# Kernel optimization log

Hardware: AMD Instinct MI355X
Metric: run time of the kernel (lower is better)

The kernel has to match this reference:

```python
import jax, jax.numpy as jnp
import numpy as np

DIM_MODEL = 1024
NUM_HEADS = 16
HEAD_DIM = DIM_MODEL // NUM_HEADS
NEG = -1000000000.0


def setup_inputs() -> dict:
    key = jax.random.key(0)
    ks = jax.random.split(key, 11)
    B, S, D = 2, 2048, DIM_MODEL
    s = 1.0 / np.sqrt(D)
    return {
        "q": jax.random.normal(ks[0], (B, S, D), jnp.float32),
        "k": jax.random.normal(ks[1], (B, S, D), jnp.float32),
        "v": jax.random.normal(ks[2], (B, S, D), jnp.float32),
        "Wq": jax.random.normal(ks[3], (D, D), jnp.float32) * s,
        "bq": jnp.zeros((D,), jnp.float32),
        "Wk": jax.random.normal(ks[4], (D, D), jnp.float32) * s,
        "bk": jnp.zeros((D,), jnp.float32),
        "Wv": jax.random.normal(ks[5], (D, D), jnp.float32) * s,
        "bv": jnp.zeros((D,), jnp.float32),
        "Wo": jax.random.normal(ks[6], (D, D), jnp.float32) * s,
        "bo": jnp.zeros((D,), jnp.float32),
    }


def reference(q, k, v, Wq, bq, Wk, bk, Wv, bv, Wo, bo):
    B, S, D = q.shape
    H, hd = NUM_HEADS, HEAD_DIM

    def proj(x, W, b):
        # torch Linear: x @ W.T + b, then split heads -> [B, H, S, hd]
        y = jnp.einsum("bsd,ed->bse", x, W) + b
        return y.reshape(B, S, H, hd).transpose(0, 2, 1, 3)

    qh = proj(q, Wq, bq)
    kh = proj(k, Wk, bk)
    vh = proj(v, Wv, bv)

    scores = jnp.einsum("bhqd,bhkd->bhqk", qh, kh) / np.sqrt(hd)
    # torch.triu(ones(S,S), diagonal=0): upper triangle INCLUDING diagonal is masked
    mask = jnp.triu(jnp.ones((S, S), bool))
    scores = jnp.where(mask, NEG, scores)
    # softmax over dim=-2 (query axis), as in the original module
    attn = jax.nn.softmax(scores, axis=-2)
    ctx = jnp.einsum("bhqk,bhkd->bhqd", attn, vh)  # [B,H,S,hd]
    ctx = ctx.transpose(0, 2, 1, 3).reshape(B, S, D)
    return jnp.einsum("bsd,ed->bse", ctx, Wo) + bo
```

## Files before the change

### kernel.cpp

```cpp
#include <hip/hip_runtime.h>

typedef __bf16 bf16;
typedef __attribute__((ext_vector_type(8))) __bf16 bf16x8;
typedef __attribute__((ext_vector_type(2))) __bf16 bf16x2;
typedef __attribute__((ext_vector_type(4))) float f32x4;

#define AS1 __attribute__((address_space(1)))
#define AS3 __attribute__((address_space(3)))

#define BB 2
#define SS 2048
#define DD 1024
#define HH 16
#define HD 64
#define BH (BB*HH)

#define QSCALE 0.1803368801111244f

static __device__ __forceinline__ f32x4 mfma16(bf16x8 a, bf16x8 b, f32x4 c) {
  return __builtin_amdgcn_mfma_f32_16x16x32_bf16(a, b, c, 0, 0, 0);
}
static __device__ __forceinline__ float fexp2(float x) {
  return __builtin_amdgcn_exp2f(x);
}

static __device__ __forceinline__ void swz1024(int bid, int& bh, int& strip0, int& qh) {
  int c = bid & 7, j = bid >> 3;
  bh = c + 8 * (j & 3);
  int rem = j >> 2;
  strip0 = rem & 15;
  qh = rem >> 4;
}

__global__ __launch_bounds__(256) void cvt_w(const float* __restrict__ s0, const float* __restrict__ s1,
                                             const float* __restrict__ s2, const float* __restrict__ s3,
                                             bf16* __restrict__ o0, bf16* __restrict__ o1,
                                             bf16* __restrict__ o2, bf16* __restrict__ o3) {
  const int z = blockIdx.y;
  const float* s = (z == 0) ? s0 : (z == 1) ? s1 : (z == 2) ? s2 : s3;
  bf16* o = (z == 0) ? o0 : (z == 1) ? o1 : (z == 2) ? o2 : o3;
  int i = blockIdx.x * 256 + threadIdx.x;
  const float4* sp = (const float4*)s;
  float4 a = sp[2 * i], b = sp[2 * i + 1];
  bf16x8 v;
  v[0] = (bf16)a.x; v[1] = (bf16)a.y; v[2] = (bf16)a.z; v[3] = (bf16)a.w;
  v[4] = (bf16)b.x; v[5] = (bf16)b.y; v[6] = (bf16)b.z; v[7] = (bf16)b.w;
  ((bf16x8*)o)[i] = v;
}

__global__ __launch_bounds__(256) void cvt_x(const float* __restrict__ s0, const float* __restrict__ s1,
                                             const float* __restrict__ s2,
                                             bf16* __restrict__ o0, bf16* __restrict__ o1,
                                             bf16* __restrict__ o2) {
  const int z = blockIdx.y;
  const float* s = (z == 0) ? s0 : (z == 1) ? s1 : s2;
  bf16* o = (z == 0) ? o0 : (z == 1) ? o1 : o2;
  int i = blockIdx.x * 256 + threadIdx.x;
  const float4* sp = (const float4*)s;
  float4 a = sp[2 * i], b = sp[2 * i + 1];
  bf16x8 v;
  v[0] = (bf16)a.x; v[1] = (bf16)a.y; v[2] = (bf16)a.z; v[3] = (bf16)a.w;
  v[4] = (bf16)b.x; v[5] = (bf16)b.y; v[6] = (bf16)b.z; v[7] = (bf16)b.w;
  ((bf16x8*)o)[i] = v;
}

__device__ __forceinline__ void gemm_core(const bf16* __restrict__ A,
                                          const bf16* __restrict__ Bm, int K,
                                          int m0, int n0, int w, int l,
                                          bf16* sA, bf16* sB, f32x4 (&acc)[4][4]) {
  const int l15 = l & 15, lg = l >> 4;
  const int wr = (w >> 1) * 64, wc = (w & 1) * 64;
  for (int kt = 0; kt < K; kt += 32) {
#pragma unroll
    for (int i = 0; i < 2; ++i) {
      int t = i * 256 + w * 64 + l;
      const bf16* ga = A + (size_t)(m0 + (t >> 2)) * K + kt + (t & 3) * 8;
      const bf16* gb = Bm + (size_t)(n0 + (t >> 2)) * K + kt + (t & 3) * 8;
      __builtin_amdgcn_global_load_lds((const AS1 void*)ga,
                                       (AS3 void*)(sA + (i * 256 + w * 64) * 8), 16, 0, 0);
      __builtin_amdgcn_global_load_lds((const AS1 void*)gb,
                                       (AS3 void*)(sB + (i * 256 + w * 64) * 8), 16, 0, 0);
    }
    __syncthreads();
    bf16x8 af[4], bfr[4];
#pragma unroll
    for (int m = 0; m < 4; ++m)
      af[m] = *(const bf16x8*)(sA + (wr + m * 16 + l15) * 32 + lg * 8);
#pragma unroll
    for (int n = 0; n < 4; ++n)
      bfr[n] = *(const bf16x8*)(sB + (wc + n * 16 + l15) * 32 + lg * 8);
#pragma unroll
    for (int m = 0; m < 4; ++m)
#pragma unroll
      for (int n = 0; n < 4; ++n)
        acc[m][n] = mfma16(af[m], bfr[n], acc[m][n]);
    __syncthreads();
  }
}

__global__ __launch_bounds__(256) void proj_gemm(
    const bf16* __restrict__ Xq, const bf16* __restrict__ Xk, const bf16* __restrict__ Xv,
    const bf16* __restrict__ Wq, const bf16* __restrict__ Wk, const bf16* __restrict__ Wv,
    const float* __restrict__ bq, const float* __restrict__ bk, const float* __restrict__ bv,
    bf16* __restrict__ Oq, bf16* __restrict__ Ok, bf16* __restrict__ Ovt) {
  __shared__ __align__(16) bf16 sA[128 * 32];
  __shared__ __align__(16) bf16 sB[128 * 32];
  const int z = blockIdx.z;
  const bf16* A = (z == 0) ? Xq : ((z == 1) ? Xk : Xv);
  const bf16* W = (z == 0) ? Wq : ((z == 1) ? Wk : Wv);
  const float* bias = (z == 0) ? bq : ((z == 1) ? bk : bv);
  const int tid = threadIdx.x, l = tid & 63, w = tid >> 6;
  const int m0 = blockIdx.y * 128, n0 = blockIdx.x * 128;
  f32x4 acc[4][4] = {};
  gemm_core(A, W, DD, m0, n0, w, l, sA, sB, acc);
  const int l15 = l & 15, lg = l >> 4;
  const int wr = (w >> 1) * 64, wc = (w & 1) * 64;
#pragma unroll
  for (int n = 0; n < 4; ++n) {
    int col = n0 + wc + n * 16 + l15;
    float bb = bias[col];
    int h = col >> 6, d = col & 63;
#pragma unroll
    for (int m = 0; m < 4; ++m) {
#pragma unroll
      for (int r = 0; r < 4; ++r) {
        int row = m0 + wr + m * 16 + lg * 4 + r;
        int b = row >> 11, s = row & (SS - 1);
        float vv = acc[m][n][r] + bb;
        if (z == 0) vv *= QSCALE;
        if (z != 2)
          ((z == 0) ? Oq : Ok)[(((size_t)(b * HH + h)) * SS + s) * HD + d] = (bf16)vv;
        else
          Ovt[(size_t)(b * HH + h) * SS * HD + ((s >> 5) * 64 + d) * 32 + (s & 31)] = (bf16)vv;
      }
    }
  }
}

__global__ __launch_bounds__(256) void out_gemm(const bf16* __restrict__ A,
                                                const bf16* __restrict__ W,
                                                const float* __restrict__ bias,
                                                float* __restrict__ out) {
  __shared__ __align__(16) bf16 sA[128 * 32];
  __shared__ __align__(16) bf16 sB[128 * 32];
  const int tid = threadIdx.x, l = tid & 63, w = tid >> 6;
  const int m0 = blockIdx.y * 128, n0 = blockIdx.x * 128;
  f32x4 acc[4][4] = {};
  gemm_core(A, W, DD, m0, n0, w, l, sA, sB, acc);
  const int l15 = l & 15, lg = l >> 4;
  const int wr = (w >> 1) * 64, wc = (w & 1) * 64;
#pragma unroll
  for (int n = 0; n < 4; ++n) {
    int col = n0 + wc + n * 16 + l15;
    float bb = bias[col];
#pragma unroll
    for (int m = 0; m < 4; ++m)
#pragma unroll
      for (int r = 0; r < 4; ++r) {
        int row = m0 + wr + m * 16 + lg * 4 + r;
        out[(size_t)row * DD + col] = acc[m][n][r] + bb;
      }
  }
}

__global__ __launch_bounds__(256) void colz(const bf16* __restrict__ Qb,
                                            const bf16* __restrict__ Kb,
                                            float* __restrict__ zPart) {
  __shared__ float zred[4][64];
  int bh, pair, qh;
  swz1024(blockIdx.x, bh, pair, qh);
  const int tid = threadIdx.x, l = tid & 63, w = tid >> 6;
  const int l15 = l & 15, lg = l >> 4;
  const bf16* Q = Qb + (size_t)bh * SS * HD;
  const bf16* Kh = Kb + (size_t)bh * SS * HD;

  for (int half = 0; half < 2; ++half) {
    const int s = half ? (31 - pair) : pair;
    const int c0 = s * 64;
    bf16x8 kf[4][2];
#pragma unroll
    for (int kt = 0; kt < 4; ++kt) {
      kf[kt][0] = *(const bf16x8*)&Kh[(c0 + kt * 16 + l15) * HD + lg * 8];
      kf[kt][1] = *(const bf16x8*)&Kh[(c0 + kt * 16 + l15) * HD + 32 + lg * 8];
    }
    float z[4] = {};
    const int qstart = c0 + qh * 64 + w * 16;
    bf16x8 qa0, qa1, qn0, qn1;
    if (qstart < SS) {
      qa0 = *(const bf16x8*)&Q[(qstart + l15) * HD + lg * 8];
      qa1 = *(const bf16x8*)&Q[(qstart + l15) * HD + 32 + lg * 8];
    }
    for (int qb = qstart; qb < SS; qb += 128) {
      const int qnext = qb + 128;
      if (qnext < SS) {
        qn0 = *(const bf16x8*)&Q[(qnext + l15) * HD + lg * 8];
        qn1 = *(const bf16x8*)&Q[(qnext + l15) * HD + 32 + lg * 8];
      }
      f32x4 d[4] = {};
#pragma unroll
      for (int kt = 0; kt < 4; ++kt) {
        d[kt] = mfma16(qa0, kf[kt][0], d[kt]);
        d[kt] = mfma16(qa1, kf[kt][1], d[kt]);
      }
#pragma unroll
      for (int kt = 0; kt < 4; ++kt) {
        const int kcol = c0 + kt * 16 + l15;
#pragma unroll
        for (int r = 0; r < 4; ++r) {
          int qq = qb + lg * 4 + r;
          z[kt] += (qq > kcol) ? fexp2(d[kt][r]) : 0.f;
        }
      }
      qa0 = qn0; qa1 = qn1;
    }
#pragma unroll
    for (int kt = 0; kt < 4; ++kt) {
      z[kt] += __shfl_xor(z[kt], 16);
      z[kt] += __shfl_xor(z[kt], 32);
    }
    if (l < 16) {
#pragma unroll
      for (int kt = 0; kt < 4; ++kt) zred[w][kt * 16 + l15] = z[kt];
    }
    __syncthreads();
    if (tid < 64) {
      float zs = zred[0][tid] + zred[1][tid] + zred[2][tid] + zred[3][tid];
      zPart[((size_t)qh * BH + bh) * SS + c0 + tid] = zs;
    }
    __syncthreads();
  }
}

__global__ __launch_bounds__(256) void rzfin(const float* __restrict__ zPart,
                                             float* __restrict__ cRZ) {
  int i = blockIdx.x * 256 + threadIdx.x;
  f32x4 a = ((const f32x4*)zPart)[i];
  f32x4 b = ((const f32x4*)(zPart + (size_t)BH * SS))[i];
  f32x4 r;
#pragma unroll
  for (int j = 0; j < 4; ++j) {
    float s = a[j] + b[j];
    r[j] = (s > 0.f) ? 1.0f / s : 0.f;
  }
  ((f32x4*)cRZ)[i] = r;
}

__global__ __launch_bounds__(256) void vscale(bf16* __restrict__ Vt,
                                              const float* __restrict__ cRZ,
                                              float* __restrict__ vlastB) {
  int i = blockIdx.x * 256 + threadIdx.x;
  int ks8 = i & 3;
  int d = (i >> 2) & 63;
  int ts = (i >> 8) & 63;
  int bh = i >> 14;
  bf16* p = Vt + ((((size_t)bh * 64 + ts) * 64 + d) * 32) + ks8 * 8;
  const float* rz = cRZ + (size_t)bh * SS + ts * 32 + ks8 * 8;
  bf16x8 v = *(const bf16x8*)p;
  if (ts == 63 && ks8 == 3) vlastB[bh * 64 + d] = (float)v[7] * (1.0f / (float)SS);
  f32x4 r0 = *(const f32x4*)rz, r1 = *(const f32x4*)(rz + 4);
  bf16x8 o;
#pragma unroll
  for (int j = 0; j < 4; ++j) o[j] = (bf16)((float)v[j] * r0[j]);
#pragma unroll
  for (int j = 0; j < 4; ++j) o[4 + j] = (bf16)((float)v[4 + j] * r1[j]);
  *(bf16x8*)p = o;
}

struct KV {
  bf16x8 k[4];
  unsigned int v[4][4];
};

static __device__ __forceinline__ void kv_load(KV& b, const bf16* __restrict__ Kh,
                                               const bf16* __restrict__ V, int k0,
                                               int l15, int lg) {
  b.k[0] = *(const bf16x8*)&Kh[(k0 + l15) * HD + lg * 8];
  b.k[1] = *(const bf16x8*)&Kh[(k0 + l15) * HD + 32 + lg * 8];
  b.k[2] = *(const bf16x8*)&Kh[(k0 + 16 + l15) * HD + lg * 8];
  b.k[3] = *(const bf16x8*)&Kh[(k0 + 16 + l15) * HD + 32 + lg * 8];
  const bf16* tile = V + ((size_t)(k0 >> 5) << 11);
#pragma unroll
  for (int dt = 0; dt < 4; ++dt) {
    const bf16* base = tile + (dt * 16 + l15) * 32;
    uint2 lo = *(const uint2*)&base[4 * lg];
    uint2 hi = *(const uint2*)&base[16 + 4 * lg];
    b.v[dt][0] = lo.x; b.v[dt][1] = lo.y; b.v[dt][2] = hi.x; b.v[dt][3] = hi.y;
  }
}

template <bool DIAG>
static __device__ __forceinline__ void kv_compute(const KV& b, int k0, int q0,
                                                  const bf16x8 (&qa)[4][2],
                                                  f32x4 (&acc)[4][4], int l15, int lg) {
  const int kb0i = k0 + lg * 4, kb1i = k0 + 16 + lg * 4;
#pragma unroll
  for (int qt = 0; qt < 4; ++qt) {
    f32x4 s0 = {}, s1 = {};
    s0 = mfma16(b.k[0], qa[qt][0], s0);
    s0 = mfma16(b.k[1], qa[qt][1], s0);
    s1 = mfma16(b.k[2], qa[qt][0], s1);
    s1 = mfma16(b.k[3], qa[qt][1], s1);
    const int qq = q0 + qt * 16 + l15;
    union { unsigned int u[4]; bf16x8 v; } pa;
#pragma unroll
    for (int hw = 0; hw < 2; ++hw) {
      bf16x2 t0, t1;
#pragma unroll
      for (int r = 0; r < 2; ++r) {
        int rr = hw * 2 + r;
        float p0 = fexp2(s0[rr]);
        float p1 = fexp2(s1[rr]);
        if (DIAG) {
          p0 = (kb0i + rr < qq) ? p0 : 0.f;
          p1 = (kb1i + rr < qq) ? p1 : 0.f;
        }
        t0[r] = (bf16)p0;
        t1[r] = (bf16)p1;
      }
      pa.u[hw] = __builtin_bit_cast(unsigned int, t0);
      pa.u[hw + 2] = __builtin_bit_cast(unsigned int, t1);
    }
#pragma unroll
    for (int dt = 0; dt < 4; ++dt) {
      union { unsigned int u[4]; bf16x8 v; } vf;
      vf.u[0] = b.v[dt][0]; vf.u[1] = b.v[dt][1];
      vf.u[2] = b.v[dt][2]; vf.u[3] = b.v[dt][3];
      acc[qt][dt] = mfma16(pa.v, vf.v, acc[qt][dt]);
    }
  }
}

__global__ __launch_bounds__(256, 2) void attn_ctx(const bf16* __restrict__ Qb,
                                                   const bf16* __restrict__ Kb,
                                                   const bf16* __restrict__ Vt,
                                                   bf16* __restrict__ ctxP0,
                                                   bf16* __restrict__ ctxP1) {
  __shared__ __align__(16) float red[2][64 * 68];
  int bh, pr, kh;
  swz1024(blockIdx.x, bh, pr, kh);
  const int tid = threadIdx.x, l = tid & 63, w = tid >> 6;
  const int l15 = l & 15, lg = l >> 4;
  const int s = kh * 4 + w;
  const bf16* Q = Qb + (size_t)bh * SS * HD;
  const bf16* Kh = Kb + (size_t)bh * SS * HD;
  const bf16* V = Vt + (size_t)bh * SS * HD;
  bf16* ctxP = kh ? ctxP1 : ctxP0;
  const int b = bh >> 4, h = bh & 15;

  for (int half = 0; half < 2; ++half) {
    const int t = half ? (31 - pr) : pr;
    const int q0 = t * 64;

    bf16x8 qa[4][2];
#pragma unroll
    for (int qt = 0; qt < 4; ++qt)
#pragma unroll
      for (int kk = 0; kk < 2; ++kk)
        qa[qt][kk] = *(const bf16x8*)&Q[(q0 + qt * 16 + l15) * HD + kk * 32 + lg * 8];

    f32x4 acc[4][4] = {};
    KV A;
    for (int k0 = s * 32; k0 < q0; k0 += 256) {
      kv_load(A, Kh, V, k0, l15, lg);
      kv_compute<false>(A, k0, q0, qa, acc, l15, lg);
    }
    {
      const int cw = (2 * t) & 7;
      int dk = (s == cw) ? q0 : ((s == ((cw + 1) & 7)) ? q0 + 32 : -1);
      if (dk >= 0) {
        kv_load(A, Kh, V, dk, l15, lg);
        kv_compute<true>(A, dk, q0, qa, acc, l15, lg);
      }
    }

    if (w == 1 || w == 3) {
      float* buf = red[(w - 1) >> 1];
#pragma unroll
      for (int qt = 0; qt < 4; ++qt)
#pragma unroll
        for (int dt = 0; dt < 4; ++dt)
          *(f32x4*)&buf[(dt * 16 + l15) * 68 + qt * 16 + lg * 4] = acc[qt][dt];
    }
    __syncthreads();
    if (w == 0 || w == 2) {
      const float* buf = red[w >> 1];
#pragma unroll
      for (int qt = 0; qt < 4; ++qt)
#pragma unroll
        for (int dt = 0; dt < 4; ++dt)
          acc[qt][dt] += *(const f32x4*)&buf[(dt * 16 + l15) * 68 + qt * 16 + lg * 4];
    }
    __syncthreads();
    if (w == 2) {
#pragma unroll
      for (int qt = 0; qt < 4; ++qt)
#pragma unroll
        for (int dt = 0; dt < 4; ++dt)
          *(f32x4*)&red[0][(dt * 16 + l15) * 68 + qt * 16 + lg * 4] = acc[qt][dt];
    }
    __syncthreads();
    if (w == 0) {
#pragma unroll
      for (int qt = 0; qt < 4; ++qt) {
#pragma unroll
        for (int dt = 0; dt < 4; ++dt) {
          f32x4 a = acc[qt][dt];
          a += *(const f32x4*)&red[0][(dt * 16 + l15) * 68 + qt * 16 + lg * 4];
#pragma unroll
          for (int r = 0; r < 4; ++r) {
            int q = q0 + qt * 16 + lg * 4 + r;
            ctxP[((size_t)(b * SS + q)) * DD + h * HD + dt * 16 + l15] = (bf16)a[r];
          }
        }
      }
    }
    __syncthreads();
  }
}

__global__ __launch_bounds__(256) void ctxfin(const bf16* __restrict__ P1,
                                              const float* __restrict__ vlastB,
                                              bf16* __restrict__ ctx) {
  int i = blockIdx.x * 256 + threadIdx.x;
  int e0 = i * 8;
  int row = e0 >> 10, col = e0 & (DD - 1);
  int b = row >> 11;
  int vidx = (b * HH + (col >> 6)) * 64 + (col & 63);
  bf16x8 p0 = ((const bf16x8*)ctx)[i];
  bf16x8 p1 = ((const bf16x8*)P1)[i];
  f32x4 v0 = *(const f32x4*)&vlastB[vidx];
  f32x4 v1 = *(const f32x4*)&vlastB[vidx + 4];
  bf16x8 o;
#pragma unroll
  for (int j = 0; j < 4; ++j) o[j] = (bf16)((float)p0[j] + (float)p1[j] + v0[j]);
#pragma unroll
  for (int j = 0; j < 4; ++j) o[4 + j] = (bf16)((float)p0[4 + j] + (float)p1[4 + j] + v1[j]);
  ((bf16x8*)ctx)[i] = o;
}

extern "C" void kernel_launch(void* const* d_in, const int* in_sizes, int n_in,
                              void* d_out, int out_size, void* d_ws, size_t ws_size,
                              hipStream_t stream) {
  const float* q  = (const float*)d_in[0];
  const float* k  = (const float*)d_in[1];
  const float* v  = (const float*)d_in[2];
  const float* Wq = (const float*)d_in[3];
  const float* bq = (const float*)d_in[4];
  const float* Wk = (const float*)d_in[5];
  const float* bk = (const float*)d_in[6];
  const float* Wv = (const float*)d_in[7];
  const float* bv = (const float*)d_in[8];
  const float* Wo = (const float*)d_in[9];
  const float* bo = (const float*)d_in[10];

  char* ws = (char*)d_ws;
  const size_t SZP = (size_t)4096 * 1024 * 2;
  const size_t SZW = (size_t)1024 * 1024 * 2;
  bf16* Qb   = (bf16*)(ws + 0 * SZP);
  bf16* Kb   = (bf16*)(ws + 1 * SZP);
  bf16* Vt   = (bf16*)(ws + 2 * SZP);
  bf16* ctxb = (bf16*)(ws + 3 * SZP);
  bf16* qb16 = (bf16*)(ws + 4 * SZP);
  bf16* kb16 = (bf16*)(ws + 5 * SZP);
  bf16* vb16 = (bf16*)(ws + 6 * SZP);
  bf16* Wqb  = (bf16*)(ws + 7 * SZP + 0 * SZW);
  bf16* Wkb  = (bf16*)(ws + 7 * SZP + 1 * SZW);
  bf16* Wvb  = (bf16*)(ws + 7 * SZP + 2 * SZW);
  bf16* Wob  = (bf16*)(ws + 7 * SZP + 3 * SZW);
  float* zPart = (float*)(ws + 7 * SZP + 4 * SZW);
  float* cRZ   = zPart + (size_t)2 * BH * SS;
  float* vlastB = cRZ + (size_t)BH * SS;
  bf16* ctxP1 = qb16;

  cvt_w<<<dim3(512, 4), 256, 0, stream>>>(Wq, Wk, Wv, Wo, Wqb, Wkb, Wvb, Wob);
  cvt_x<<<dim3(2048, 3), 256, 0, stream>>>(q, k, v, qb16, kb16, vb16);

  proj_gemm<<<dim3(1024 / 128, 4096 / 128, 3), 256, 0, stream>>>(
      qb16, kb16, vb16, Wqb, Wkb, Wvb, bq, bk, bv, Qb, Kb, Vt);

  colz<<<1024, 256, 0, stream>>>(Qb, Kb, zPart);
  rzfin<<<(BH * SS / 4) / 256, 256, 0, stream>>>(zPart, cRZ);
  vscale<<<(BH * HD * SS / 8) / 256, 256, 0, stream>>>(Vt, cRZ, vlastB);
  attn_ctx<<<1024, 256, 0, stream>>>(Qb, Kb, Vt, ctxb, ctxP1);
  ctxfin<<<(4096 * 1024 / 8) / 256, 256, 0, stream>>>(ctxP1, vlastB, ctxb);

  out_gemm<<<dim3(1024 / 128, 4096 / 128), 256, 0, stream>>>(ctxb, Wob, bo, (float*)d_out);
}
```

Before: 168.2 us.

## Share K/V chunks via LDS across waves and split keys four ways

The attention kernel changes from per-wave private K/V register loads with a shared-memory cross-wave reduction to a 128-query tile. Each wave owns 32 query rows, and the block stages each 32-key K/V chunk into LDS with global_load_lds so all four waves reuse it. The key range is now split across four blocks instead of two, writing four partial context buffers that ctxfin sums. This removes the LDS reduction and cuts redundant global K/V loads. In exchange it adds two barriers per chunk, one more partial buffer to write and read, and reuses the kb16/vb16 scratch buffers as partial outputs.

Result: no change. 169.3 us (+0.7%).

```diff
diff --git a/kernel.cpp b/kernel.cpp
--- a/kernel.cpp
+++ b/kernel.cpp
@@ -24,12 +24,12 @@
   return __builtin_amdgcn_exp2f(x);
 }
 
-static __device__ __forceinline__ void swz1024(int bid, int& bh, int& strip0, int& qh) {
+static __device__ __forceinline__ void swz1024(int bid, int& bh, int& a, int& b2) {
   int c = bid & 7, j = bid >> 3;
   bh = c + 8 * (j & 3);
   int rem = j >> 2;
-  strip0 = rem & 15;
-  qh = rem >> 4;
+  a = rem & 15;
+  b2 = rem >> 4;
 }
 
 __global__ __launch_bounds__(256) void cvt_w(const float* __restrict__ s0, const float* __restrict__ s1,
@@ -266,42 +266,33 @@
   *(bf16x8*)p = o;
 }
 
-struct KV {
-  bf16x8 k[4];
-  unsigned int v[4][4];
-};
-
-static __device__ __forceinline__ void kv_load(KV& b, const bf16* __restrict__ Kh,
-                                               const bf16* __restrict__ V, int k0,
-                                               int l15, int lg) {
-  b.k[0] = *(const bf16x8*)&Kh[(k0 + l15) * HD + lg * 8];
-  b.k[1] = *(const bf16x8*)&Kh[(k0 + l15) * HD + 32 + lg * 8];
-  b.k[2] = *(const bf16x8*)&Kh[(k0 + 16 + l15) * HD + lg * 8];
-  b.k[3] = *(const bf16x8*)&Kh[(k0 + 16 + l15) * HD + 32 + lg * 8];
-  const bf16* tile = V + ((size_t)(k0 >> 5) << 11);
+template <bool DIAG>
+static __device__ __forceinline__ void chunk_compute(
+    const bf16* sKe, const bf16* sVe, int k0, int qw,
+    const bf16x8 (&qa)[2][2], f32x4 (&acc)[2][4], int l15, int lg) {
+  bf16x8 kf00 = *(const bf16x8*)(sKe + l15 * 32 + lg * 8);
+  bf16x8 kf01 = *(const bf16x8*)(sKe + 1024 + l15 * 32 + lg * 8);
+  bf16x8 kf10 = *(const bf16x8*)(sKe + (16 + l15) * 32 + lg * 8);
+  bf16x8 kf11 = *(const bf16x8*)(sKe + 1024 + (16 + l15) * 32 + lg * 8);
+  union U { unsigned int u[4]; bf16x8 v; };
+  U vf[4];
 #pragma unroll
   for (int dt = 0; dt < 4; ++dt) {
-    const bf16* base = tile + (dt * 16 + l15) * 32;
+    const bf16* base = sVe + (dt * 16 + l15) * 32;
     uint2 lo = *(const uint2*)&base[4 * lg];
     uint2 hi = *(const uint2*)&base[16 + 4 * lg];
-    b.v[dt][0] = lo.x; b.v[dt][1] = lo.y; b.v[dt][2] = hi.x; b.v[dt][3] = hi.y;
-  }
-}
-
-template <bool DIAG>
-static __device__ __forceinline__ void kv_compute(const KV& b, int k0, int q0,
-                                                  const bf16x8 (&qa)[4][2],
-                                                  f32x4 (&acc)[4][4], int l15, int lg) {
+    vf[dt].u[0] = lo.x; vf[dt].u[1] = lo.y; vf[dt].u[2] = hi.x; vf[dt].u[3] = hi.y;
+  }
   const int kb0i = k0 + lg * 4, kb1i = k0 + 16 + lg * 4;
 #pragma unroll
-  for (int qt = 0; qt < 4; ++qt) {
+  for (int qt = 0; qt < 2; ++qt) {
     f32x4 s0 = {}, s1 = {};
-    s0 = mfma16(b.k[0], qa[qt][0], s0);
-    s0 = mfma16(b.k[1], qa[qt][1], s0);
-    s1 = mfma16(b.k[2], qa[qt][0], s1);
-    s1 = mfma16(b.k[3], qa[qt][1], s1);
-    const int qq = q0 + qt * 16 + l15;
-    union { unsigned int u[4]; bf16x8 v; } pa;
+    s0 = mfma16(kf00, qa[qt][0], s0);
+    s0 = mfma16(kf01, qa[qt][1], s0);
+    s1 = mfma16(kf10, qa[qt][0], s1);
+    s1 = mfma16(kf11, qa[qt][1], s1);
+    const int qq = qw + qt * 16 + l15;
+    U pa;
 #pragma unroll
     for (int hw = 0; hw < 2; ++hw) {
       bf16x2 t0, t1;
@@ -321,104 +312,79 @@
       pa.u[hw + 2] = __builtin_bit_cast(unsigned int, t1);
     }
 #pragma unroll
-    for (int dt = 0; dt < 4; ++dt) {
-      union { unsigned int u[4]; bf16x8 v; } vf;
-      vf.u[0] = b.v[dt][0]; vf.u[1] = b.v[dt][1];
-      vf.u[2] = b.v[dt][2]; vf.u[3] = b.v[dt][3];
-      acc[qt][dt] = mfma16(pa.v, vf.v, acc[qt][dt]);
-    }
+    for (int dt = 0; dt < 4; ++dt)
+      acc[qt][dt] = mfma16(pa.v, vf[dt].v, acc[qt][dt]);
   }
 }
 
 __global__ __launch_bounds__(256, 2) void attn_ctx(const bf16* __restrict__ Qb,
                                                    const bf16* __restrict__ Kb,
                                                    const bf16* __restrict__ Vt,
-                                                   bf16* __restrict__ ctxP0,
-                                                   bf16* __restrict__ ctxP1) {
-  __shared__ __align__(16) float red[2][64 * 68];
-  int bh, pr, kh;
-  swz1024(blockIdx.x, bh, pr, kh);
+                                                   bf16* __restrict__ P0,
+                                                   bf16* __restrict__ P1,
+                                                   bf16* __restrict__ P2,
+                                                   bf16* __restrict__ P3) {
+  __shared__ __align__(16) bf16 sK[2 * 32 * 32];
+  __shared__ __align__(16) bf16 sV[64 * 32];
+  int bh, a, b2;
+  swz1024(blockIdx.x, bh, a, b2);
+  const int pr = a & 7;
+  const int j = (b2 << 1) | (a >> 3);
   const int tid = threadIdx.x, l = tid & 63, w = tid >> 6;
   const int l15 = l & 15, lg = l >> 4;
-  const int s = kh * 4 + w;
   const bf16* Q = Qb + (size_t)bh * SS * HD;
   const bf16* Kh = Kb + (size_t)bh * SS * HD;
   const bf16* V = Vt + (size_t)bh * SS * HD;
-  bf16* ctxP = kh ? ctxP1 : ctxP0;
+  bf16* ctxP = (j == 0) ? P0 : (j == 1) ? P1 : (j == 2) ? P2 : P3;
   const int b = bh >> 4, h = bh & 15;
 
+  const int skk = tid >> 7, sr = (tid >> 2) & 31, sc = tid & 3;
+  bf16* dK = sK + (size_t)w * 512;
+  bf16* dV = sV + (size_t)w * 512;
+
   for (int half = 0; half < 2; ++half) {
-    const int t = half ? (31 - pr) : pr;
-    const int q0 = t * 64;
-
-    bf16x8 qa[4][2];
-#pragma unroll
-    for (int qt = 0; qt < 4; ++qt)
+    const int T = half ? (15 - pr) : pr;
+    const int q0 = T * 128;
+    const int qw = q0 + w * 32;
+
+    bf16x8 qa[2][2];
+#pragma unroll
+    for (int qt = 0; qt < 2; ++qt)
 #pragma unroll
       for (int kk = 0; kk < 2; ++kk)
-        qa[qt][kk] = *(const bf16x8*)&Q[(q0 + qt * 16 + l15) * HD + kk * 32 + lg * 8];
-
-    f32x4 acc[4][4] = {};
-    KV A;
-    for (int k0 = s * 32; k0 < q0; k0 += 256) {
-      kv_load(A, Kh, V, k0, l15, lg);
-      kv_compute<false>(A, k0, q0, qa, acc, l15, lg);
-    }
-    {
-      const int cw = (2 * t) & 7;
-      int dk = (s == cw) ? q0 : ((s == ((cw + 1) & 7)) ? q0 + 32 : -1);
-      if (dk >= 0) {
-        kv_load(A, Kh, V, dk, l15, lg);
-        kv_compute<true>(A, dk, q0, qa, acc, l15, lg);
-      }
-    }
-
-    if (w == 1 || w == 3) {
-      float* buf = red[(w - 1) >> 1];
-#pragma unroll
-      for (int qt = 0; qt < 4; ++qt)
+        qa[qt][kk] = *(const bf16x8*)&Q[(qw + qt * 16 + l15) * HD + kk * 32 + lg * 8];
+
+    f32x4 acc[2][4] = {};
+    const int kend = q0 + 128;
+    for (int k0 = j * 32; k0 < kend; k0 += 128) {
+      const bf16* gK = Kh + (size_t)(k0 + sr) * HD + skk * 32 + sc * 8;
+      const bf16* gV = V + (((size_t)(k0 >> 5)) << 11) + tid * 8;
+      __builtin_amdgcn_global_load_lds((const AS1 void*)gK, (AS3 void*)dK, 16, 0, 0);
+      __builtin_amdgcn_global_load_lds((const AS1 void*)gV, (AS3 void*)dV, 16, 0, 0);
+      __syncthreads();
+      if (k0 < qw)
+        chunk_compute<false>(sK, sV, k0, qw, qa, acc, l15, lg);
+      else if (k0 == qw)
+        chunk_compute<true>(sK, sV, k0, qw, qa, acc, l15, lg);
+      __syncthreads();
+    }
+
+#pragma unroll
+    for (int qt = 0; qt < 2; ++qt)
+#pragma unroll
+      for (int r = 0; r < 4; ++r) {
+        int q = qw + qt * 16 + lg * 4 + r;
 #pragma unroll
         for (int dt = 0; dt < 4; ++dt)
-          *(f32x4*)&buf[(dt * 16 + l15) * 68 + qt * 16 + lg * 4] = acc[qt][dt];
-    }
-    __syncthreads();
-    if (w == 0 || w == 2) {
-      const float* buf = red[w >> 1];
-#pragma unroll
-      for (int qt = 0; qt < 4; ++qt)
-#pragma unroll
-        for (int dt = 0; dt < 4; ++dt)
-          acc[qt][dt] += *(const f32x4*)&buf[(dt * 16 + l15) * 68 + qt * 16 + lg * 4];
-    }
-    __syncthreads();
-    if (w == 2) {
-#pragma unroll
-      for (int qt = 0; qt < 4; ++qt)
-#pragma unroll
-        for (int dt = 0; dt < 4; ++dt)
-          *(f32x4*)&red[0][(dt * 16 + l15) * 68 + qt * 16 + lg * 4] = acc[qt][dt];
-    }
-    __syncthreads();
-    if (w == 0) {
-#pragma unroll
-      for (int qt = 0; qt < 4; ++qt) {
-#pragma unroll
-        for (int dt = 0; dt < 4; ++dt) {
-          f32x4 a = acc[qt][dt];
-          a += *(const f32x4*)&red[0][(dt * 16 + l15) * 68 + qt * 16 + lg * 4];
-#pragma unroll
-          for (int r = 0; r < 4; ++r) {
-            int q = q0 + qt * 16 + lg * 4 + r;
-            ctxP[((size_t)(b * SS + q)) * DD + h * HD + dt * 16 + l15] = (bf16)a[r];
-          }
-        }
-      }
-    }
-    __syncthreads();
+          ctxP[((size_t)(b * SS + q)) * DD + h * HD + dt * 16 + l15] =
+              (bf16)acc[qt][dt][r];
+      }
   }
 }
 
 __global__ __launch_bounds__(256) void ctxfin(const bf16* __restrict__ P1,
+                                              const bf16* __restrict__ P2,
+                                              const bf16* __restrict__ P3,
                                               const float* __restrict__ vlastB,
                                               bf16* __restrict__ ctx) {
   int i = blockIdx.x * 256 + threadIdx.x;
@@ -428,13 +394,18 @@
   int vidx = (b * HH + (col >> 6)) * 64 + (col & 63);
   bf16x8 p0 = ((const bf16x8*)ctx)[i];
   bf16x8 p1 = ((const bf16x8*)P1)[i];
+  bf16x8 p2 = ((const bf16x8*)P2)[i];
+  bf16x8 p3 = ((const bf16x8*)P3)[i];
   f32x4 v0 = *(const f32x4*)&vlastB[vidx];
   f32x4 v1 = *(const f32x4*)&vlastB[vidx + 4];
   bf16x8 o;
 #pragma unroll
-  for (int j = 0; j < 4; ++j) o[j] = (bf16)((float)p0[j] + (float)p1[j] + v0[j]);
-#pragma unroll
-  for (int j = 0; j < 4; ++j) o[4 + j] = (bf16)((float)p0[4 + j] + (float)p1[4 + j] + v1[j]);
+  for (int jj = 0; jj < 4; ++jj)
+    o[jj] = (bf16)(((float)p0[jj] + (float)p1[jj]) + ((float)p2[jj] + (float)p3[jj]) + v0[jj]);
+#pragma unroll
+  for (int jj = 0; jj < 4; ++jj)
+    o[4 + jj] = (bf16)(((float)p0[4 + jj] + (float)p1[4 + jj]) +
+                       ((float)p2[4 + jj] + (float)p3[4 + jj]) + v1[jj]);
   ((bf16x8*)ctx)[i] = o;
 }
 
@@ -470,7 +441,6 @@
   float* zPart = (float*)(ws + 7 * SZP + 4 * SZW);
   float* cRZ   = zPart + (size_t)2 * BH * SS;
   float* vlastB = cRZ + (size_t)BH * SS;
-  bf16* ctxP1 = qb16;
 
   cvt_w<<<dim3(512, 4), 256, 0, stream>>>(Wq, Wk, Wv, Wo, Wqb, Wkb, Wvb, Wob);
   cvt_x<<<dim3(2048, 3), 256, 0, stream>>>(q, k, v, qb16, kb16, vb16);
@@ -481,8 +451,8 @@
   colz<<<1024, 256, 0, stream>>>(Qb, Kb, zPart);
   rzfin<<<(BH * SS / 4) / 256, 256, 0, stream>>>(zPart, cRZ);
   vscale<<<(BH * HD * SS / 8) / 256, 256, 0, stream>>>(Vt, cRZ, vlastB);
-  attn_ctx<<<1024, 256, 0, stream>>>(Qb, Kb, Vt, ctxb, ctxP1);
-  ctxfin<<<(4096 * 1024 / 8) / 256, 256, 0, stream>>>(ctxP1, vlastB, ctxb);
+  attn_ctx<<<1024, 256, 0, stream>>>(Qb, Kb, Vt, ctxb, qb16, kb16, vb16);
+  ctxfin<<<(4096 * 1024 / 8) / 256, 256, 0, stream>>>(qb16, kb16, vb16, vlastB, ctxb);
 
   out_gemm<<<dim3(1024 / 128, 4096 / 128), 256, 0, stream>>>(ctxb, Wob, bo, (float*)d_out);
 }
```
